# Kernel optimization log

Measured on AMD Instinct MI355X. Metric: run time of the kernel, lower is better.

## Reference

```python
import jax, jax.numpy as jnp
import numpy as np

# dims
B, C, N, E = 2048, 3, 32, 256       # batch, views, keypoints, embed_dim
H, L, MLP, P = 8, 3, 1024, 256      # heads, blocks (depth-1), mlp hidden, proj_dim
VIS_KP = 16                          # visible keypoints per sample (constant, as the torch code assumes)
K = VIS_KP + 1                       # + always-visible view token
HD = E // H
SCALE = HD ** -0.5


def _sinusoidal_pe(n, d):
    pos = np.arange(n)[:, None].astype(np.float32)
    i = np.arange(d)[None, :]
    ang = pos / np.power(10000.0, (2 * (i // 2)) / d)
    pe = np.where(i % 2 == 0, np.sin(ang), np.cos(ang))
    return jnp.asarray(pe, dtype=jnp.float32)

PE = _sinusoidal_pe(N, E)  # (N, E)


def layer_norm(x, s, b, eps=1e-5):
    mu = jnp.mean(x, -1, keepdims=True)
    var = jnp.var(x, -1, keepdims=True)
    return (x - mu) * jax.lax.rsqrt(var + eps) * s + b


def _heads(t, T):
    return t.reshape(-1, T, H, HD).transpose(0, 2, 1, 3)  # (S,H,T,HD)


def _gelu(x):
    return jax.nn.gelu(x, approximate=False)


def _mha(x, qkv_w, qkv_b, pw, pb):
    T = x.shape[1]
    q, k, v = jnp.split(x @ qkv_w + qkv_b, 3, axis=-1)
    q, k, v = _heads(q, T), _heads(k, T), _heads(v, T)
    a = jax.nn.softmax(jnp.einsum('shtd,shud->shtu', q, k) * SCALE, -1)
    o = jnp.einsum('shtu,shud->shtd', a, v).transpose(0, 2, 1, 3).reshape(-1, T, E)
    return o @ pw + pb


def reference(x, occlusion_mask, kp_w, kp_b, view_tokens, view_pos,
              ln1_s, ln1_b, qkv_w, qkv_b, ap_w, ap_b, ln2_s, ln2_b,
              fc1_w, fc1_b, fc2_w, fc2_b,
              pool_probe, pool_ln1_s, pool_ln1_b, pool_q_w, pool_q_b,
              pool_kv_w, pool_kv_b, pool_ap_w, pool_ap_b,
              pool_ln2_s, pool_ln2_b, pool_fc1_w, pool_fc1_b,
              pool_fc2_w, pool_fc2_b, pool_out_w, pool_out_b, last_s, last_b):
    # keypoint embedding + sinusoidal positional encoding
    xe = x.reshape(B * C, N, 2) @ kp_w + kp_b + PE[None]
    xe = xe.reshape(B, C, N, E)
    # prepend learnable view tokens (+ view positional embedding)
    vt = jnp.broadcast_to(view_tokens + view_pos, (B, C, 1, E))
    xt = jnp.concatenate([vt, xe], axis=2).reshape(B * C, N + 1, E)
    mask = jnp.concatenate([jnp.ones((B, C, 1, 1), bool), occlusion_mask], axis=2)
    mask = mask.reshape(B * C, N + 1)
    # stream compaction: gather the K visible tokens per sample, order-preserving
    order = jnp.argsort(jnp.where(mask, 0, 1).astype(jnp.int32), axis=1)[:, :K]
    vis = jnp.take_along_axis(xt, order[:, :, None], axis=1)  # (B*C, K, E)
    # pre-norm transformer blocks
    for l in range(L):
        y = vis + _mha(layer_norm(vis, ln1_s[l], ln1_b[l]), qkv_w[l], qkv_b[l], ap_w[l], ap_b[l])
        h = _gelu(layer_norm(y, ln2_s[l], ln2_b[l]) @ fc1_w[l] + fc1_b[l]) @ fc2_w[l] + fc2_b[l]
        vis = y + h
    # attention pooling: learnable probe cross-attends to the sequence
    probe = jnp.broadcast_to(pool_probe, (B * C, 1, E))
    kn = layer_norm(vis, pool_ln1_s, pool_ln1_b)
    q = _heads(probe @ pool_q_w + pool_q_b, 1)
    kk, vv = jnp.split(kn @ pool_kv_w + pool_kv_b, 2, axis=-1)
    kk, vv = _heads(kk, K), _heads(vv, K)
    a = jax.nn.softmax(jnp.einsum('shqd,shkd->shqk', q, kk) * SCALE, -1)
    o = jnp.einsum('shqk,shkd->shqd', a, vv).transpose(0, 2, 1, 3).reshape(B * C, 1, E)
    y = probe + o @ pool_ap_w + pool_ap_b
    y = y + _gelu(layer_norm(y, pool_ln2_s, pool_ln2_b) @ pool_fc1_w + pool_fc1_b) @ pool_fc2_w + pool_fc2_b
    out = (y @ pool_out_w + pool_out_b).reshape(B, C, P)
    return layer_norm(out, last_s, last_b)


def setup_inputs() -> dict:
    key = jax.random.key(0)
    ks = iter(jax.random.split(key, 64))

    def rn(shape, scale=0.02):
        return jax.random.normal(next(ks), shape, jnp.float32) * scale

    x = jax.random.normal(next(ks), (B, C, N, 2), jnp.float32)
    # exactly VIS_KP visible keypoints per sample (torch code assumes constant count)
    rng = np.random.default_rng(0)
    r = rng.random((B, C, N))
    rank = np.argsort(np.argsort(r, axis=-1), axis=-1)
    occlusion_mask = jnp.asarray((rank < VIS_KP)[..., None])
    return dict(
        x=x, occlusion_mask=occlusion_mask,
        kp_w=rn((2, E)), kp_b=jnp.zeros((E,)),
        view_tokens=rn((1, C, 1, E)), view_pos=rn((1, C, 1, E)),
        ln1_s=jnp.ones((L, E)), ln1_b=jnp.zeros((L, E)),
        qkv_w=rn((L, E, 3 * E)), qkv_b=jnp.zeros((L, 3 * E)),
        ap_w=rn((L, E, E)), ap_b=jnp.zeros((L, E)),
        ln2_s=jnp.ones((L, E)), ln2_b=jnp.zeros((L, E)),
        fc1_w=rn((L, E, MLP)), fc1_b=jnp.zeros((L, MLP)),
        fc2_w=rn((L, MLP, E)), fc2_b=jnp.zeros((L, E)),
        pool_probe=rn((1, 1, E)),
        pool_ln1_s=jnp.ones((E,)), pool_ln1_b=jnp.zeros((E,)),
        pool_q_w=rn((E, E)), pool_q_b=jnp.zeros((E,)),
        pool_kv_w=rn((E, 2 * E)), pool_kv_b=jnp.zeros((2 * E,)),
        pool_ap_w=rn((E, E)), pool_ap_b=jnp.zeros((E,)),
        pool_ln2_s=jnp.ones((E,)), pool_ln2_b=jnp.zeros((E,)),
        pool_fc1_w=rn((E, MLP)), pool_fc1_b=jnp.zeros((MLP,)),
        pool_fc2_w=rn((MLP, E)), pool_fc2_b=jnp.zeros((E,)),
        pool_out_w=rn((E, P)), pool_out_b=jnp.zeros((P,)),
        last_s=jnp.ones((P,)), last_b=jnp.zeros((P,)),
    )
```

## Files before the change

### kernel.cpp

```cpp
#include <hip/hip_runtime.h>
#include <hip/hip_bf16.h>
#include <math.h>


#define NB   2048
#define NC   3
#define NN   32
#define NE   256
#define NH   8
#define HDIM 32
#define NL   3
#define NMLP 1024
#define NP   256
#define NK   17
#define NR   (2*NK)
#define NS   (NB*NC)
#define NBLK (NS/2)
#define NT   512
#define NW   8
#define AST  264
#define BHS  520
#define BVS  260

#define SZ_QKV  589824
#define SZ_AP   196608
#define SZ_FC1  786432
#define SZ_FC2  786432
#define SZ_KV   131072
#define OFF_QKV 0
#define OFF_AP  (OFF_QKV + SZ_QKV)
#define OFF_FC1 (OFF_AP + SZ_AP)
#define OFF_FC2 (OFF_FC1 + SZ_FC1)
#define OFF_KV  (OFF_FC2 + SZ_FC2)
#define WTOT    (OFF_KV + SZ_KV)
#define WS_NEEDED ((size_t)WTOT * 2 * 2)

typedef unsigned short u16;
typedef __attribute__((ext_vector_type(8))) short short8;
typedef __attribute__((ext_vector_type(4))) float float4v;

struct Params {
  const void* x; const void* mask;
  const void* kp_w; const void* kp_b;
  const void* view_tokens; const void* view_pos;
  const void* ln1_s; const void* ln1_b;
  const void* qkv_w; const void* qkv_b;
  const void* ap_w; const void* ap_b;
  const void* ln2_s; const void* ln2_b;
  const void* fc1_w; const void* fc1_b;
  const void* fc2_w; const void* fc2_b;
  const void* pool_probe;
  const void* pool_ln1_s; const void* pool_ln1_b;
  const void* pool_q_w; const void* pool_q_b;
  const void* pool_kv_w; const void* pool_kv_b;
  const void* pool_ap_w; const void* pool_ap_b;
  const void* pool_ln2_s; const void* pool_ln2_b;
  const void* pool_fc1_w; const void* pool_fc1_b;
  const void* pool_fc2_w; const void* pool_fc2_b;
  const void* pool_out_w; const void* pool_out_b;
  const void* last_s; const void* last_b;
  float* out;
  u16* ws;
};

__device__ __forceinline__ float b2f(u16 u) {
  return __uint_as_float(((unsigned)u) << 16);
}
__device__ __forceinline__ u16 cvt16(float v) {
  return __bfloat16_as_ushort(__float2bfloat16(v));
}
__device__ __forceinline__ float geluf(float v) {
  return 0.5f * v * (1.0f + erff(v * 0.70710678118654752f));
}
template <bool BF>
__device__ __forceinline__ float LD(const void* q, int i) {
  if constexpr (BF) return b2f(((const u16*)q)[i]);
  else return ((const float*)q)[i];
}
__device__ __forceinline__ float4v vzero() {
  float4v z; z[0] = 0.f; z[1] = 0.f; z[2] = 0.f; z[3] = 0.f; return z;
}

template <bool BF>
__device__ void prep_body(const Params& p, int idx) {
  size_t i = idx, src; const void* W;
  if (i < SZ_QKV) {
    const size_t l = i / 196608, r = i % 196608, n = r / 256, k = r % 256;
    W = p.qkv_w; src = l * 196608 + k * 768 + n;
  } else if ((i -= SZ_QKV) < SZ_AP) {
    const size_t l = i / 65536, r = i % 65536, n = r / 256, k = r % 256;
    W = p.ap_w; src = l * 65536 + k * 256 + n;
  } else if ((i -= SZ_AP) < SZ_FC1) {
    const size_t l = i / 262144, r = i % 262144, n = r / 256, k = r % 256;
    W = p.fc1_w; src = l * 262144 + k * 1024 + n;
  } else if ((i -= SZ_FC1) < SZ_FC2) {
    const size_t l = i / 262144, r = i % 262144, n = r / 1024, k = r % 1024;
    W = p.fc2_w; src = l * 262144 + k * 256 + n;
  } else {
    i -= SZ_FC2;
    const size_t n = i / 256, k = i % 256;
    W = p.pool_kv_w; src = k * 512 + n;
  }
  u16 hi, lo;
  if constexpr (BF) {
    hi = ((const u16*)W)[src]; lo = 0;
  } else {
    const float wv = ((const float*)W)[src];
    hi = cvt16(wv);
    lo = cvt16(wv - b2f(hi));
  }
  p.ws[idx] = hi;
  p.ws[WTOT + idx] = lo;
}

__global__ __launch_bounds__(256)
void prep_kernel(Params p) {
  const int idx = blockIdx.x * 256 + threadIdx.x;
  if (idx >= WTOT) return;
  const bool isbf = (((const u16*)p.ln1_s)[0] == 0x3F80);
  if (isbf) prep_body<true>(p, idx);
  else      prep_body<false>(p, idx);
}

struct alignas(16) Smem {
  float X[NR][NE];
  u16  Ahi[NR * AST];
  u16  Alo[NR * AST];
  u16  Bh[NR * BHS];
  float Bv[NR][BVS];
  float Q[2][NE];
  float O[2][NE];
  float RowA[2][NE];
  float Pp[2][NH][NK];
  float Red[NW];
  int  Idx[2][NK];
};

template <bool BF>
__device__ __forceinline__ void ln_hl(const float* __restrict__ In,
                                      u16* __restrict__ Oh, u16* __restrict__ Ol,
                                      const void* __restrict__ gam,
                                      const void* __restrict__ bet) {
  const int lane = threadIdx.x & 63, w = threadIdx.x >> 6;
  for (int t = w; t < NR; t += NW) {
    const float* row = In + t * NE;
    float sum = 0.f, sq = 0.f;
#pragma unroll
    for (int kk = 0; kk < NE / 64; ++kk) {
      const float v = row[lane + 64 * kk];
      sum += v; sq += v * v;
    }
#pragma unroll
    for (int off = 32; off > 0; off >>= 1) {
      sum += __shfl_down(sum, off, 64);
      sq  += __shfl_down(sq,  off, 64);
    }
    sum = __shfl(sum, 0, 64);
    sq  = __shfl(sq,  0, 64);
    const float mu = sum * (1.0f / NE);
    const float r  = rsqrtf(sq * (1.0f / NE) - mu * mu + 1e-5f);
#pragma unroll
    for (int kk = 0; kk < NE / 64; ++kk) {
      const int k = lane + 64 * kk;
      const float v = (row[k] - mu) * r * LD<BF>(gam, k) + LD<BF>(bet, k);
      const u16 hv = cvt16(v);
      Oh[t * AST + k] = hv;
      Ol[t * AST + k] = cvt16(v - b2f(hv));
    }
  }
}

template <bool BF>
__device__ __forceinline__ void tile9(const short8 f0h, const short8 f0l,
                                      const short8 f1h, const short8 f1l,
                                      const short8 a2h, const short8 a2l,
                                      const short8 bh, const short8 bl,
                                      float4v& D0, float4v& D1, float4v& D2) {
  D0 = __builtin_amdgcn_mfma_f32_16x16x32_bf16(f0h, bh, D0, 0, 0, 0);
  D1 = __builtin_amdgcn_mfma_f32_16x16x32_bf16(f1h, bh, D1, 0, 0, 0);
  D2 = __builtin_amdgcn_mfma_f32_16x16x32_bf16(a2h, bh, D2, 0, 0, 0);
  D0 = __builtin_amdgcn_mfma_f32_16x16x32_bf16(f0l, bh, D0, 0, 0, 0);
  D1 = __builtin_amdgcn_mfma_f32_16x16x32_bf16(f1l, bh, D1, 0, 0, 0);
  D2 = __builtin_amdgcn_mfma_f32_16x16x32_bf16(a2l, bh, D2, 0, 0, 0);
  if constexpr (!BF) {
    D0 = __builtin_amdgcn_mfma_f32_16x16x32_bf16(f0h, bl, D0, 0, 0, 0);
    D1 = __builtin_amdgcn_mfma_f32_16x16x32_bf16(f1h, bl, D1, 0, 0, 0);
    D2 = __builtin_amdgcn_mfma_f32_16x16x32_bf16(a2h, bl, D2, 0, 0, 0);
  }
}

template <bool BF, int KS, int KST>
__device__ __forceinline__ void mfmaD_ws(const u16* __restrict__ Ah,
                                         const u16* __restrict__ Al,
                                         const int ast,
                                         const u16* __restrict__ Wh,
                                         const u16* __restrict__ Wl,
                                         const int koff,
                                         const int n0, const int n1,
                                         float4v& D0a, float4v& D1a, float4v& D2a,
                                         float4v& D0b, float4v& D1b, float4v& D2b) {
  const int lane = threadIdx.x & 63;
  const int col = lane & 15, quad = lane >> 4;
  const u16* __restrict__ b0h = Wh + (size_t)n0 * KST + koff + quad * 8;
  const u16* __restrict__ b0l = Wl + (size_t)n0 * KST + koff + quad * 8;
  const u16* __restrict__ b1h = Wh + (size_t)n1 * KST + koff + quad * 8;
  const u16* __restrict__ b1l = Wl + (size_t)n1 * KST + koff + quad * 8;
  const short8 z8 = {0, 0, 0, 0, 0, 0, 0, 0};
#pragma unroll
  for (int ks = 0; ks < KS; ++ks) {
    const int k0 = ks * 32 + quad * 8;
    const short8 bh0 = *(const short8*)(b0h + ks * 32);
    const short8 bh1 = *(const short8*)(b1h + ks * 32);
    short8 bl0 = z8, bl1 = z8;
    if constexpr (!BF) {
      bl0 = *(const short8*)(b0l + ks * 32);
      bl1 = *(const short8*)(b1l + ks * 32);
    }
    const short8 f0h = *(const short8*)(Ah + col * ast + k0);
    const short8 f0l = *(const short8*)(Al + col * ast + k0);
    const short8 f1h = *(const short8*)(Ah + (16 + col) * ast + k0);
    const short8 f1l = *(const short8*)(Al + (16 + col) * ast + k0);
    short8 a2h = z8, a2l = z8;
    if (col < 2) {
      a2h = *(const short8*)(Ah + (32 + col) * ast + k0);
      a2l = *(const short8*)(Al + (32 + col) * ast + k0);
    }
    tile9<BF>(f0h, f0l, f1h, f1l, a2h, a2l, bh0, bl0, D0a, D1a, D2a);
    tile9<BF>(f0h, f0l, f1h, f1l, a2h, a2l, bh1, bl1, D0b, D1b, D2b);
  }
}

template <bool BF, int KS, int KST>
__device__ __forceinline__ void mfmaT_ws(const u16* __restrict__ Ah,
                                         const u16* __restrict__ Al,
                                         const int ast,
                                         const u16* __restrict__ Wh,
                                         const u16* __restrict__ Wl,
                                         const int koff,
                                         const int n0, const int n1, const int n2,
                                         float4v& D0a, float4v& D1a, float4v& D2a,
                                         float4v& D0b, float4v& D1b, float4v& D2b,
                                         float4v& D0c, float4v& D1c, float4v& D2c) {
  const int lane = threadIdx.x & 63;
  const int col = lane & 15, quad = lane >> 4;
  const u16* __restrict__ b0h = Wh + (size_t)n0 * KST + koff + quad * 8;
  const u16* __restrict__ b0l = Wl + (size_t)n0 * KST + koff + quad * 8;
  const u16* __restrict__ b1h = Wh + (size_t)n1 * KST + koff + quad * 8;
  const u16* __restrict__ b1l = Wl + (size_t)n1 * KST + koff + quad * 8;
  const u16* __restrict__ b2h = Wh + (size_t)n2 * KST + koff + quad * 8;
  const u16* __restrict__ b2l = Wl + (size_t)n2 * KST + koff + quad * 8;
  const short8 z8 = {0, 0, 0, 0, 0, 0, 0, 0};
#pragma unroll
  for (int ks = 0; ks < KS; ++ks) {
    const int k0 = ks * 32 + quad * 8;
    const short8 f0h = *(const short8*)(Ah + col * ast + k0);
    const short8 f0l = *(const short8*)(Al + col * ast + k0);
    const short8 f1h = *(const short8*)(Ah + (16 + col) * ast + k0);
    const short8 f1l = *(const short8*)(Al + (16 + col) * ast + k0);
    short8 a2h = z8, a2l = z8;
    if (col < 2) {
      a2h = *(const short8*)(Ah + (32 + col) * ast + k0);
      a2l = *(const short8*)(Al + (32 + col) * ast + k0);
    }
    {
      const short8 bh0 = *(const short8*)(b0h + ks * 32);
      const short8 bh1 = *(const short8*)(b1h + ks * 32);
      short8 bl0 = z8, bl1 = z8;
      if constexpr (!BF) {
        bl0 = *(const short8*)(b0l + ks * 32);
        bl1 = *(const short8*)(b1l + ks * 32);
      }
      tile9<BF>(f0h, f0l, f1h, f1l, a2h, a2l, bh0, bl0, D0a, D1a, D2a);
      tile9<BF>(f0h, f0l, f1h, f1l, a2h, a2l, bh1, bl1, D0b, D1b, D2b);
    }
    {
      const short8 bh2 = *(const short8*)(b2h + ks * 32);
      short8 bl2 = z8;
      if constexpr (!BF) bl2 = *(const short8*)(b2l + ks * 32);
      tile9<BF>(f0h, f0l, f1h, f1l, a2h, a2l, bh2, bl2, D0c, D1c, D2c);
    }
  }
}

template <bool BF, int KS>
__device__ __forceinline__ void mfma1_in(const u16* __restrict__ Ah,
                                         const u16* __restrict__ Al,
                                         const int ast,
                                         const void* __restrict__ W, const int wN,
                                         const int koff, const int n,
                                         float4v& D0, float4v& D1, float4v& D2) {
  const int lane = threadIdx.x & 63;
  const int col = lane & 15, quad = lane >> 4;
  const short8 z8 = {0, 0, 0, 0, 0, 0, 0, 0};
  for (int ks = 0; ks < KS; ++ks) {
    const int k0 = ks * 32 + quad * 8;
    const short8 f0h = *(const short8*)(Ah + col * ast + k0);
    const short8 f0l = *(const short8*)(Al + col * ast + k0);
    const short8 f1h = *(const short8*)(Ah + (16 + col) * ast + k0);
    const short8 f1l = *(const short8*)(Al + (16 + col) * ast + k0);
    short8 a2h = z8, a2l = z8;
    if (col < 2) {
      a2h = *(const short8*)(Ah + (32 + col) * ast + k0);
      a2l = *(const short8*)(Al + (32 + col) * ast + k0);
    }
    short8 bh, bl = z8;
#pragma unroll
    for (int j2 = 0; j2 < 8; ++j2) {
      const size_t off = (size_t)(koff + k0 + j2) * wN + n;
      if constexpr (BF) {
        bh[j2] = (short)((const u16*)W)[off];
      } else {
        const float wv = ((const float*)W)[off];
        const u16 hv = cvt16(wv);
        bh[j2] = (short)hv;
        bl[j2] = (short)cvt16(wv - b2f(hv));
      }
    }
    tile9<BF>(f0h, f0l, f1h, f1l, a2h, a2l, bh, bl, D0, D1, D2);
  }
}

__device__ __forceinline__ float group_sum(float v, float* sRed, int sid) {
#pragma unroll
  for (int off = 32; off > 0; off >>= 1) v += __shfl_down(v, off, 64);
  __syncthreads();
  if ((threadIdx.x & 63) == 0) sRed[threadIdx.x >> 6] = v;
  __syncthreads();
  return sRed[sid * 4 + 0] + sRed[sid * 4 + 1] +
         sRed[sid * 4 + 2] + sRed[sid * 4 + 3];
}

template <bool BF, bool WS>
__device__ void body(const Params& p, Smem& sm) {
  const int s0  = blockIdx.x * 2;
  const int tid = threadIdx.x;
  const size_t EB = BF ? 2 : 4;
  const int lane = tid & 63, wv_ = tid >> 6, col = lane & 15, quad = lane >> 4;
  const u16* wsh = p.ws;
  const u16* wsl = p.ws + WTOT;
  u16* Hhi = sm.Bh;
  u16* Hlo = (u16*)&sm.Bv[0][0];

  if (tid < 2) {
    const int sid = tid, sg = s0 + sid;
    const unsigned int* mw = (const unsigned int*)p.mask;
    bool byte_layout = false;
    for (int i = 0; i < 8; ++i) {
      const unsigned int w = mw[i];
      if (w != 0u && w != 1u && w != 0x3F800000u) { byte_layout = true; break; }
    }
    int np_ = 0;
    sm.Idx[sid][np_++] = -1;
    if (byte_layout) {
      const unsigned char* mb = (const unsigned char*)p.mask;
      for (int n = 0; n < NN && np_ < NK; ++n)
        if (mb[(size_t)sg * NN + n]) sm.Idx[sid][np_++] = n;
    } else {
      for (int n = 0; n < NN && np_ < NK; ++n)
        if (mw[(size_t)sg * NN + n] != 0u) sm.Idx[sid][np_++] = n;
    }
    while (np_ < NK) sm.Idx[sid][np_++] = 0;
  }
  __syncthreads();

  {
    const int e  = tid & (NE - 1);
    const int th = tid >> 8;
    const float kw0 = LD<BF>(p.kp_w, e);
    const float kw1 = LD<BF>(p.kp_w, NE + e);
    const float kb  = LD<BF>(p.kp_b, e);
    const int   i2  = e & ~1;
    const float freq = expf(-((float)i2 / (float)NE) * logf(10000.0f));
    for (int g = th; g < NR; g += 2) {
      const int sid = (g >= NK) ? 1 : 0;
      const int t   = g - sid * NK;
      const int sg  = s0 + sid;
      const int c   = sg % NC;
      const int n   = sm.Idx[sid][t];
      float v;
      if (n < 0) {
        v = LD<BF>(p.view_tokens, c * NE + e) + LD<BF>(p.view_pos, c * NE + e);
      } else {
        const float x0 = LD<BF>(p.x, (sg * NN + n) * 2 + 0);
        const float x1 = LD<BF>(p.x, (sg * NN + n) * 2 + 1);
        const float ang = (float)n * freq;
        const float pe  = (e & 1) ? cosf(ang) : sinf(ang);
        v = x0 * kw0 + x1 * kw1 + kb + pe;
      }
      sm.X[g][e] = v;
    }
  }
  __syncthreads();

#pragma unroll 1
  for (int l = 0; l < NL; ++l) {
    const void* qkvw = (const char*)p.qkv_w + (size_t)l * NE * 3 * NE * EB;
    const void* qkvb = (const char*)p.qkv_b + (size_t)l * 3 * NE * EB;
    const void* apw  = (const char*)p.ap_w  + (size_t)l * NE * NE * EB;
    const void* apb  = (const char*)p.ap_b  + (size_t)l * NE * EB;
    const void* f1w  = (const char*)p.fc1_w + (size_t)l * NE * NMLP * EB;
    const void* f1b  = (const char*)p.fc1_b + (size_t)l * NMLP * EB;
    const void* f2w  = (const char*)p.fc2_w + (size_t)l * NMLP * NE * EB;
    const void* f2bb = (const char*)p.fc2_b + (size_t)l * NE * EB;

    ln_hl<BF>(&sm.X[0][0], sm.Ahi, sm.Alo,
              (const char*)p.ln1_s + (size_t)l * NE * EB,
              (const char*)p.ln1_b + (size_t)l * NE * EB);
    __syncthreads();

    {
      auto wb_qkv = [&](int n, float4v D0, float4v D1, float4v D2) {
        const float bb = LD<BF>(qkvb, n);
#pragma unroll
        for (int r = 0; r < 4; ++r) {
          const int g0 = quad * 4 + r;
          const int g1 = 16 + quad * 4 + r;
          const int g2 = 32 + quad * 4 + r;
          if (n < 512) {
            sm.Bh[g0 * BHS + n] = cvt16(D0[r] + bb);
            sm.Bh[g1 * BHS + n] = cvt16(D1[r] + bb);
            if (g2 < NR) sm.Bh[g2 * BHS + n] = cvt16(D2[r] + bb);
          } else {
            sm.Bv[g0][n - 512] = D0[r] + bb;
            sm.Bv[g1][n - 512] = D1[r] + bb;
            if (g2 < NR) sm.Bv[g2][n - 512] = D2[r] + bb;
          }
        }
      };
#pragma unroll 1
      for (int pass = 0; pass < 2; ++pass) {
        const int n0 = (wv_ + (pass * 3 + 0) * NW) * 16 + col;
        const int n1 = (wv_ + (pass * 3 + 1) * NW) * 16 + col;
        const int n2 = (wv_ + (pass * 3 + 2) * NW) * 16 + col;
        float4v D0a = vzero(), D1a = vzero(), D2a = vzero();
        float4v D0b = vzero(), D1b = vzero(), D2b = vzero();
        float4v D0c = vzero(), D1c = vzero(), D2c = vzero();
        if constexpr (WS)
          mfmaT_ws<BF, 8, 256>(sm.Ahi, sm.Alo, AST,
                               wsh + OFF_QKV + (size_t)l * 196608,
                               wsl + OFF_QKV + (size_t)l * 196608, 0,
                               n0, n1, n2,
                               D0a, D1a, D2a, D0b, D1b, D2b, D0c, D1c, D2c);
        else {
          mfma1_in<BF, 8>(sm.Ahi, sm.Alo, AST, qkvw, 3 * NE, 0, n0, D0a, D1a, D2a);
          mfma1_in<BF, 8>(sm.Ahi, sm.Alo, AST, qkvw, 3 * NE, 0, n1, D0b, D1b, D2b);
          mfma1_in<BF, 8>(sm.Ahi, sm.Alo, AST, qkvw, 3 * NE, 0, n2, D0c, D1c, D2c);
        }
        wb_qkv(n0, D0a, D1a, D2a);
        wb_qkv(n1, D0b, D1b, D2b);
        wb_qkv(n2, D0c, D1c, D2c);
      }
    }
    __syncthreads();

    if (tid < 2 * NH * NK) {
      const int sid = tid / (NH * NK);
      const int rem = tid - sid * (NH * NK);
      const int h = rem / NK, t = rem % NK;
      const int gb = sid * NK;
      float q[HDIM];
#pragma unroll
      for (int i8 = 0; i8 < HDIM / 8; ++i8) {
        const short8 qq = *(const short8*)&sm.Bh[(gb + t) * BHS + h * HDIM + i8 * 8];
#pragma unroll
        for (int j = 0; j < 8; ++j) q[i8 * 8 + j] = b2f((u16)qq[j]);
      }
      float sc[NK];
      float mx = -1e30f;
#pragma unroll
      for (int u = 0; u < NK; ++u) {
        float d = 0.f;
#pragma unroll
        for (int i8 = 0; i8 < HDIM / 8; ++i8) {
          const short8 kk = *(const short8*)&sm.Bh[(gb + u) * BHS + 256 + h * HDIM + i8 * 8];
#pragma unroll
          for (int j = 0; j < 8; ++j) d += q[i8 * 8 + j] * b2f((u16)kk[j]);
        }
        d *= 0.17677669529663687f;
        sc[u] = d;
        mx = fmaxf(mx, d);
      }
      float den = 0.f;
#pragma unroll
      for (int u = 0; u < NK; ++u) { sc[u] = __expf(sc[u] - mx); den += sc[u]; }
      const float inv = 1.0f / den;
#pragma unroll
      for (int u = 0; u < NK; ++u) sc[u] *= inv;
#pragma unroll
      for (int i4 = 0; i4 < HDIM / 4; ++i4) {
        float4v o = vzero();
#pragma unroll
        for (int u = 0; u < NK; ++u) {
          const float4v vv = *(const float4v*)&sm.Bv[gb + u][h * HDIM + i4 * 4];
          o[0] += sc[u] * vv[0];
          o[1] += sc[u] * vv[1];
          o[2] += sc[u] * vv[2];
          o[3] += sc[u] * vv[3];
        }
#pragma unroll
        for (int r = 0; r < 4; ++r) {
          const int jc = h * HDIM + i4 * 4 + r;
          const u16 hv = cvt16(o[r]);
          sm.Ahi[(gb + t) * AST + jc] = hv;
          sm.Alo[(gb + t) * AST + jc] = cvt16(o[r] - b2f(hv));
        }
      }
    }
    __syncthreads();

    {
      auto wb_proj = [&](int n, float4v D0, float4v D1, float4v D2) {
        const float bb = LD<BF>(apb, n);
#pragma unroll
        for (int r = 0; r < 4; ++r) {
          const int g0 = quad * 4 + r;
          const int g1 = 16 + quad * 4 + r;
          const int g2 = 32 + quad * 4 + r;
          sm.X[g0][n] = sm.X[g0][n] + D0[r] + bb;
          sm.X[g1][n] = sm.X[g1][n] + D1[r] + bb;
          if (g2 < NR) sm.X[g2][n] = sm.X[g2][n] + D2[r] + bb;
        }
      };
      const int n0 = wv_ * 16 + col;
      const int n1 = (wv_ + NW) * 16 + col;
      float4v D0a = vzero(), D1a = vzero(), D2a = vzero();
      float4v D0b = vzero(), D1b = vzero(), D2b = vzero();
      if constexpr (WS)
        mfmaD_ws<BF, 8, 256>(sm.Ahi, sm.Alo, AST,
                             wsh + OFF_AP + (size_t)l * 65536,
                             wsl + OFF_AP + (size_t)l * 65536, 0, n0, n1,
                             D0a, D1a, D2a, D0b, D1b, D2b);
      else {
        mfma1_in<BF, 8>(sm.Ahi, sm.Alo, AST, apw, NE, 0, n0, D0a, D1a, D2a);
        mfma1_in<BF, 8>(sm.Ahi, sm.Alo, AST, apw, NE, 0, n1, D0b, D1b, D2b);
      }
      wb_proj(n0, D0a, D1a, D2a);
      wb_proj(n1, D0b, D1b, D2b);
    }
    __syncthreads();

    ln_hl<BF>(&sm.X[0][0], sm.Ahi, sm.Alo,
              (const char*)p.ln2_s + (size_t)l * NE * EB,
              (const char*)p.ln2_b + (size_t)l * NE * EB);
    __syncthreads();

#pragma unroll 1
    for (int chunk = 0; chunk < 2; ++chunk) {
      {
        auto wb_fc1 = [&](int n, float4v D0, float4v D1, float4v D2) {
          const float bb = LD<BF>(f1b, chunk * 512 + n);
#pragma unroll
          for (int r = 0; r < 4; ++r) {
            const int g0 = quad * 4 + r;
            const int g1 = 16 + quad * 4 + r;
            const int g2 = 32 + quad * 4 + r;
            {
              const float v = geluf(D0[r] + bb);
              const u16 hv = cvt16(v);
              Hhi[g0 * BHS + n] = hv;
              Hlo[g0 * BHS + n] = cvt16(v - b2f(hv));
            }
            {
              const float v = geluf(D1[r] + bb);
              const u16 hv = cvt16(v);
              Hhi[g1 * BHS + n] = hv;
              Hlo[g1 * BHS + n] = cvt16(v - b2f(hv));
            }
            if (g2 < NR) {
              const float v = geluf(D2[r] + bb);
              const u16 hv = cvt16(v);
              Hhi[g2 * BHS + n] = hv;
              Hlo[g2 * BHS + n] = cvt16(v - b2f(hv));
            }
          }
        };
#pragma unroll 1
        for (int pass = 0; pass < 2; ++pass) {
          const int n0 = (wv_ + (pass * 2 + 0) * NW) * 16 + col;
          const int n1 = (wv_ + (pass * 2 + 1) * NW) * 16 + col;
          float4v D0a = vzero(), D1a = vzero(), D2a = vzero();
          float4v D0b = vzero(), D1b = vzero(), D2b = vzero();
          if constexpr (WS)
            mfmaD_ws<BF, 8, 256>(sm.Ahi, sm.Alo, AST,
                                 wsh + OFF_FC1 + (size_t)l * 262144 + (size_t)chunk * 131072,
                                 wsl + OFF_FC1 + (size_t)l * 262144 + (size_t)chunk * 131072,
                                 0, n0, n1, D0a, D1a, D2a, D0b, D1b, D2b);
          else {
            const void* f1wc = (const char*)f1w + (size_t)chunk * 512 * EB;
            mfma1_in<BF, 8>(sm.Ahi, sm.Alo, AST, f1wc, NMLP, 0, n0, D0a, D1a, D2a);
            mfma1_in<BF, 8>(sm.Ahi, sm.Alo, AST, f1wc, NMLP, 0, n1, D0b, D1b, D2b);
          }
          wb_fc1(n0, D0a, D1a, D2a);
          wb_fc1(n1, D0b, D1b, D2b);
        }
      }
      __syncthreads();
      {
        auto wb_fc2 = [&](int n, float4v D0, float4v D1, float4v D2) {
          const float bb = (chunk == 0) ? LD<BF>(f2bb, n) : 0.f;
#pragma unroll
          for (int r = 0; r < 4; ++r) {
            const int g0 = quad * 4 + r;
            const int g1 = 16 + quad * 4 + r;
            const int g2 = 32 + quad * 4 + r;
            sm.X[g0][n] = sm.X[g0][n] + D0[r] + bb;
            sm.X[g1][n] = sm.X[g1][n] + D1[r] + bb;
            if (g2 < NR) sm.X[g2][n] = sm.X[g2][n] + D2[r] + bb;
          }
        };
        const int n0 = wv_ * 16 + col;
        const int n1 = (wv_ + NW) * 16 + col;
        float4v D0a = vzero(), D1a = vzero(), D2a = vzero();
        float4v D0b = vzero(), D1b = vzero(), D2b = vzero();
        if constexpr (WS)
          mfmaD_ws<BF, 16, 1024>(Hhi, Hlo, BHS,
                                 wsh + OFF_FC2 + (size_t)l * 262144,
                                 wsl + OFF_FC2 + (size_t)l * 262144,
                                 chunk * 512, n0, n1,
                                 D0a, D1a, D2a, D0b, D1b, D2b);
        else {
          mfma1_in<BF, 16>(Hhi, Hlo, BHS, f2w, NE, chunk * 512, n0, D0a, D1a, D2a);
          mfma1_in<BF, 16>(Hhi, Hlo, BHS, f2w, NE, chunk * 512, n1, D0b, D1b, D2b);
        }
        wb_fc2(n0, D0a, D1a, D2a);
        wb_fc2(n1, D0b, D1b, D2b);
      }
      __syncthreads();
    }
  }

  ln_hl<BF>(&sm.X[0][0], sm.Ahi, sm.Alo, p.pool_ln1_s, p.pool_ln1_b);
  __syncthreads();
  const int sid = tid >> 8;
  const int j   = tid & (NE - 1);
  {
    float a = LD<BF>(p.pool_q_b, j);
#pragma unroll 4
    for (int k = 0; k < NE; k += 4) {
      a += LD<BF>(p.pool_probe, k + 0) * LD<BF>(p.pool_q_w, (k + 0) * NE + j) +
           LD<BF>(p.pool_probe, k + 1) * LD<BF>(p.pool_q_w, (k + 1) * NE + j) +
           LD<BF>(p.pool_probe, k + 2) * LD<BF>(p.pool_q_w, (k + 2) * NE + j) +
           LD<BF>(p.pool_probe, k + 3) * LD<BF>(p.pool_q_w, (k + 3) * NE + j);
    }
    sm.Q[sid][j] = a;
  }
  {
    auto wb_kv = [&](int n, float4v D0, float4v D1, float4v D2) {
      const float bb = LD<BF>(p.pool_kv_b, n);
#pragma unroll
      for (int r = 0; r < 4; ++r) {
        const int g0 = quad * 4 + r;
        const int g1 = 16 + quad * 4 + r;
        const int g2 = 32 + quad * 4 + r;
        if (n < 256) {
          sm.Bh[g0 * BHS + n] = cvt16(D0[r] + bb);
          sm.Bh[g1 * BHS + n] = cvt16(D1[r] + bb);
          if (g2 < NR) sm.Bh[g2 * BHS + n] = cvt16(D2[r] + bb);
        } else {
          sm.Bv[g0][n - 256] = D0[r] + bb;
          sm.Bv[g1][n - 256] = D1[r] + bb;
          if (g2 < NR) sm.Bv[g2][n - 256] = D2[r] + bb;
        }
      }
    };
#pragma unroll 1
    for (int pass = 0; pass < 2; ++pass) {
      const int n0 = (wv_ + (pass * 2 + 0) * NW) * 16 + col;
      const int n1 = (wv_ + (pass * 2 + 1) * NW) * 16 + col;
      float4v D0a = vzero(), D1a = vzero(), D2a = vzero();
      float4v D0b = vzero(), D1b = vzero(), D2b = vzero();
      if constexpr (WS)
        mfmaD_ws<BF, 8, 256>(sm.Ahi, sm.Alo, AST, wsh + OFF_KV, wsl + OFF_KV,
                             0, n0, n1, D0a, D1a, D2a, D0b, D1b, D2b);
      else {
        mfma1_in<BF, 8>(sm.Ahi, sm.Alo, AST, p.pool_kv_w, 2 * NE, 0, n0, D0a, D1a, D2a);
        mfma1_in<BF, 8>(sm.Ahi, sm.Alo, AST, p.pool_kv_w, 2 * NE, 0, n1, D0b, D1b, D2b);
      }
      wb_kv(n0, D0a, D1a, D2a);
      wb_kv(n1, D0b, D1b, D2b);
    }
  }
  __syncthreads();
  if (tid < 2 * NH) {
    const int ps = tid >> 3, h = tid & 7;
    const int gb = ps * NK;
    float sc[NK];
    float mx = -1e30f;
#pragma unroll
    for (int u = 0; u < NK; ++u) {
      float d = 0.f;
#pragma unroll
      for (int i8 = 0; i8 < HDIM / 8; ++i8) {
        const short8 kk = *(const short8*)&sm.Bh[(gb + u) * BHS + h * HDIM + i8 * 8];
#pragma unroll
        for (int jx = 0; jx < 8; ++jx)
          d += sm.Q[ps][h * HDIM + i8 * 8 + jx] * b2f((u16)kk[jx]);
      }
      d *= 0.17677669529663687f;
      sc[u] = d;
      mx = fmaxf(mx, d);
    }
    float den = 0.f;
#pragma unroll
    for (int u = 0; u < NK; ++u) { sc[u] = __expf(sc[u] - mx); den += sc[u]; }
    const float inv = 1.0f / den;
#pragma unroll
    for (int u = 0; u < NK; ++u) sm.Pp[ps][h][u] = sc[u] * inv;
  }
  __syncthreads();
  {
    const int h = j >> 5, i = j & 31;
    float o = 0.f;
#pragma unroll
    for (int u = 0; u < NK; ++u)
      o += sm.Pp[sid][h][u] * sm.Bv[sid * NK + u][h * HDIM + i];
    sm.O[sid][j] = o;
  }
  __syncthreads();
  float yv;
  {
    float a = LD<BF>(p.pool_ap_b, j);
#pragma unroll 4
    for (int k = 0; k < NE; k += 4) {
      const float4 oo = *(const float4*)&sm.O[sid][k];
      a += oo.x * LD<BF>(p.pool_ap_w, (k + 0) * NE + j) +
           oo.y * LD<BF>(p.pool_ap_w, (k + 1) * NE + j) +
           oo.z * LD<BF>(p.pool_ap_w, (k + 2) * NE + j) +
           oo.w * LD<BF>(p.pool_ap_w, (k + 3) * NE + j);
    }
    yv = LD<BF>(p.pool_probe, j) + a;
  }
  {
    const float s1 = group_sum(yv, sm.Red, sid);
    const float s2 = group_sum(yv * yv, sm.Red, sid);
    const float mu = s1 * (1.0f / NE);
    const float r  = rsqrtf(s2 * (1.0f / NE) - mu * mu + 1e-5f);
    sm.Q[sid][j] = (yv - mu) * r * LD<BF>(p.pool_ln2_s, j) + LD<BF>(p.pool_ln2_b, j);
  }
  __syncthreads();
  float* Hh = (float*)&sm.Bv[0][0];
  {
    float h1[4];
#pragma unroll
    for (int c4 = 0; c4 < 4; ++c4) h1[c4] = LD<BF>(p.pool_fc1_b, c4 * NE + j);
#pragma unroll 4
    for (int k = 0; k < NE; k += 4) {
      const float4 nq = *(const float4*)&sm.Q[sid][k];
#pragma unroll
      for (int c4 = 0; c4 < 4; ++c4) {
        const int cjj = c4 * NE + j;
        h1[c4] += nq.x * LD<BF>(p.pool_fc1_w, (k + 0) * NMLP + cjj) +
                  nq.y * LD<BF>(p.pool_fc1_w, (k + 1) * NMLP + cjj) +
                  nq.z * LD<BF>(p.pool_fc1_w, (k + 2) * NMLP + cjj) +
                  nq.w * LD<BF>(p.pool_fc1_w, (k + 3) * NMLP + cjj);
      }
    }
    __syncthreads();
#pragma unroll
    for (int c4 = 0; c4 < 4; ++c4) Hh[sid * NMLP + c4 * NE + j] = geluf(h1[c4]);
  }
  __syncthreads();
  {
    float a = LD<BF>(p.pool_fc2_b, j);
#pragma unroll 4
    for (int k = 0; k < NMLP; k += 4) {
      const float4 hh = *(const float4*)&Hh[sid * NMLP + k];
      a += hh.x * LD<BF>(p.pool_fc2_w, (k + 0) * NE + j) +
           hh.y * LD<BF>(p.pool_fc2_w, (k + 1) * NE + j) +
           hh.z * LD<BF>(p.pool_fc2_w, (k + 2) * NE + j) +
           hh.w * LD<BF>(p.pool_fc2_w, (k + 3) * NE + j);
    }
    yv += a;
    sm.RowA[sid][j] = yv;
  }
  __syncthreads();
  float ov;
  {
    float a = LD<BF>(p.pool_out_b, j);
#pragma unroll 4
    for (int k = 0; k < NE; k += 4) {
      const float4 yy = *(const float4*)&sm.RowA[sid][k];
      a += yy.x * LD<BF>(p.pool_out_w, (k + 0) * NP + j) +
           yy.y * LD<BF>(p.pool_out_w, (k + 1) * NP + j) +
           yy.z * LD<BF>(p.pool_out_w, (k + 2) * NP + j) +
           yy.w * LD<BF>(p.pool_out_w, (k + 3) * NP + j);
    }
    ov = a;
  }
  {
    const float s1 = group_sum(ov, sm.Red, sid);
    const float s2 = group_sum(ov * ov, sm.Red, sid);
    const float mu = s1 * (1.0f / NP);
    const float r  = rsqrtf(s2 * (1.0f / NP) - mu * mu + 1e-5f);
    const float res = (ov - mu) * r * LD<BF>(p.last_s, j) + LD<BF>(p.last_b, j);
    p.out[(size_t)(s0 + sid) * NP + j] = res;
  }
}

__global__ __launch_bounds__(NT)
__attribute__((amdgpu_waves_per_eu(2, 2)))
void st_encoder_ws(Params p) {
  __shared__ Smem sm;
  const bool isbf = (((const u16*)p.ln1_s)[0] == 0x3F80);
  if (isbf) body<true, true>(p, sm);
  else      body<false, true>(p, sm);
}

__global__ __launch_bounds__(NT)
__attribute__((amdgpu_waves_per_eu(2, 2)))
void st_encoder_nows(Params p) {
  __shared__ Smem sm;
  const bool isbf = (((const u16*)p.ln1_s)[0] == 0x3F80);
  if (isbf) body<true, false>(p, sm);
  else      body<false, false>(p, sm);
}

extern "C" void kernel_launch(void* const* d_in, const int* in_sizes, int n_in,
                              void* d_out, int out_size, void* d_ws, size_t ws_size,
                              hipStream_t stream) {
  (void)in_sizes; (void)n_in; (void)out_size;
  Params p;
  p.x           = d_in[0];
  p.mask        = d_in[1];
  p.kp_w        = d_in[2];
  p.kp_b        = d_in[3];
  p.view_tokens = d_in[4];
  p.view_pos    = d_in[5];
  p.ln1_s       = d_in[6];
  p.ln1_b       = d_in[7];
  p.qkv_w       = d_in[8];
  p.qkv_b       = d_in[9];
  p.ap_w        = d_in[10];
  p.ap_b        = d_in[11];
  p.ln2_s       = d_in[12];
  p.ln2_b       = d_in[13];
  p.fc1_w       = d_in[14];
  p.fc1_b       = d_in[15];
  p.fc2_w       = d_in[16];
  p.fc2_b       = d_in[17];
  p.pool_probe  = d_in[18];
  p.pool_ln1_s  = d_in[19];
  p.pool_ln1_b  = d_in[20];
  p.pool_q_w    = d_in[21];
  p.pool_q_b    = d_in[22];
  p.pool_kv_w   = d_in[23];
  p.pool_kv_b   = d_in[24];
  p.pool_ap_w   = d_in[25];
  p.pool_ap_b   = d_in[26];
  p.pool_ln2_s  = d_in[27];
  p.pool_ln2_b  = d_in[28];
  p.pool_fc1_w  = d_in[29];
  p.pool_fc1_b  = d_in[30];
  p.pool_fc2_w  = d_in[31];
  p.pool_fc2_b  = d_in[32];
  p.pool_out_w  = d_in[33];
  p.pool_out_b  = d_in[34];
  p.last_s      = d_in[35];
  p.last_b      = d_in[36];
  p.out         = (float*)d_out;
  p.ws          = (u16*)d_ws;
  if (d_ws != nullptr && ws_size >= WS_NEEDED) {
    prep_kernel<<<dim3((WTOT + 255) / 256), dim3(256), 0, stream>>>(p);
    st_encoder_ws<<<dim3(NBLK), dim3(NT), 0, stream>>>(p);
  } else {
    st_encoder_nows<<<dim3(NBLK), dim3(NT), 0, stream>>>(p);
  }
}
```

Baseline: 5.257 ms.

## Double block size to 1024 threads and split MFMA tiles across sixteen waves

Raises threads per block from 512 to 1024 (16 waves) and redistributes the QKV, projection, FC1, FC2 and pool KV MFMA column tiles so each wave does one pass instead of two. A new single-column MFMA helper is added for the projection and FC2 stages. The pooling tail keeps its 512-thread mapping and guards the upper half of the block as inactive. The waves_per_eu hint is removed. The intent is more in-flight waves per block to hide latency, at the cost of higher register pressure per thread and idle waves during pooling.

```diff
diff --git a/kernel.cpp b/kernel.cpp
--- a/kernel.cpp
+++ b/kernel.cpp
@@ -16,8 +16,8 @@
 #define NR   (2*NK)
 #define NS   (NB*NC)
 #define NBLK (NS/2)
-#define NT   512
-#define NW   8
+#define NT   1024
+#define NW   16
 #define AST  264
 #define BHS  520
 #define BVS  260
@@ -190,6 +190,38 @@
 }
 
 template <bool BF, int KS, int KST>
+__device__ __forceinline__ void mfmaS_ws(const u16* __restrict__ Ah,
+                                         const u16* __restrict__ Al,
+                                         const int ast,
+                                         const u16* __restrict__ Wh,
+                                         const u16* __restrict__ Wl,
+                                         const int koff, const int n,
+                                         float4v& D0, float4v& D1, float4v& D2) {
+  const int lane = threadIdx.x & 63;
+  const int col = lane & 15, quad = lane >> 4;
+  const u16* __restrict__ b0h = Wh + (size_t)n * KST + koff + quad * 8;
+  const u16* __restrict__ b0l = Wl + (size_t)n * KST + koff + quad * 8;
+  const short8 z8 = {0, 0, 0, 0, 0, 0, 0, 0};
+#pragma unroll
+  for (int ks = 0; ks < KS; ++ks) {
+    const int k0 = ks * 32 + quad * 8;
+    const short8 bh0 = *(const short8*)(b0h + ks * 32);
+    short8 bl0 = z8;
+    if constexpr (!BF) bl0 = *(const short8*)(b0l + ks * 32);
+    const short8 f0h = *(const short8*)(Ah + col * ast + k0);
+    const short8 f0l = *(const short8*)(Al + col * ast + k0);
+    const short8 f1h = *(const short8*)(Ah + (16 + col) * ast + k0);
+    const short8 f1l = *(const short8*)(Al + (16 + col) * ast + k0);
+    short8 a2h = z8, a2l = z8;
+    if (col < 2) {
+      a2h = *(const short8*)(Ah + (32 + col) * ast + k0);
+      a2l = *(const short8*)(Al + (32 + col) * ast + k0);
+    }
+    tile9<BF>(f0h, f0l, f1h, f1l, a2h, a2l, bh0, bl0, D0, D1, D2);
+  }
+}
+
+template <bool BF, int KS, int KST>
 __device__ __forceinline__ void mfmaD_ws(const u16* __restrict__ Ah,
                                          const u16* __restrict__ Al,
                                          const int ast,
@@ -326,8 +358,8 @@
   __syncthreads();
   if ((threadIdx.x & 63) == 0) sRed[threadIdx.x >> 6] = v;
   __syncthreads();
-  return sRed[sid * 4 + 0] + sRed[sid * 4 + 1] +
-         sRed[sid * 4 + 2] + sRed[sid * 4 + 3];
+  const int b = (sid & 1) * 4;
+  return sRed[b + 0] + sRed[b + 1] + sRed[b + 2] + sRed[b + 3];
 }
 
 template <bool BF, bool WS>
@@ -371,7 +403,7 @@
     const float kb  = LD<BF>(p.kp_b, e);
     const int   i2  = e & ~1;
     const float freq = expf(-((float)i2 / (float)NE) * logf(10000.0f));
-    for (int g = th; g < NR; g += 2) {
+    for (int g = th; g < NR; g += 4) {
       const int sid = (g >= NK) ? 1 : 0;
       const int t   = g - sid * NK;
       const int sg  = s0 + sid;
@@ -427,29 +459,26 @@
           }
         }
       };
-#pragma unroll 1
-      for (int pass = 0; pass < 2; ++pass) {
-        const int n0 = (wv_ + (pass * 3 + 0) * NW) * 16 + col;
-        const int n1 = (wv_ + (pass * 3 + 1) * NW) * 16 + col;
-        const int n2 = (wv_ + (pass * 3 + 2) * NW) * 16 + col;
-        float4v D0a = vzero(), D1a = vzero(), D2a = vzero();
-        float4v D0b = vzero(), D1b = vzero(), D2b = vzero();
-        float4v D0c = vzero(), D1c = vzero(), D2c = vzero();
-        if constexpr (WS)
-          mfmaT_ws<BF, 8, 256>(sm.Ahi, sm.Alo, AST,
-                               wsh + OFF_QKV + (size_t)l * 196608,
-                               wsl + OFF_QKV + (size_t)l * 196608, 0,
-                               n0, n1, n2,
-                               D0a, D1a, D2a, D0b, D1b, D2b, D0c, D1c, D2c);
-        else {
-          mfma1_in<BF, 8>(sm.Ahi, sm.Alo, AST, qkvw, 3 * NE, 0, n0, D0a, D1a, D2a);
-          mfma1_in<BF, 8>(sm.Ahi, sm.Alo, AST, qkvw, 3 * NE, 0, n1, D0b, D1b, D2b);
-          mfma1_in<BF, 8>(sm.Ahi, sm.Alo, AST, qkvw, 3 * NE, 0, n2, D0c, D1c, D2c);
-        }
-        wb_qkv(n0, D0a, D1a, D2a);
-        wb_qkv(n1, D0b, D1b, D2b);
-        wb_qkv(n2, D0c, D1c, D2c);
-      }
+      const int n0 = (wv_ + 0 * NW) * 16 + col;
+      const int n1 = (wv_ + 1 * NW) * 16 + col;
+      const int n2 = (wv_ + 2 * NW) * 16 + col;
+      float4v D0a = vzero(), D1a = vzero(), D2a = vzero();
+      float4v D0b = vzero(), D1b = vzero(), D2b = vzero();
+      float4v D0c = vzero(), D1c = vzero(), D2c = vzero();
+      if constexpr (WS)
+        mfmaT_ws<BF, 8, 256>(sm.Ahi, sm.Alo, AST,
+                             wsh + OFF_QKV + (size_t)l * 196608,
+                             wsl + OFF_QKV + (size_t)l * 196608, 0,
+                             n0, n1, n2,
+                             D0a, D1a, D2a, D0b, D1b, D2b, D0c, D1c, D2c);
+      else {
+        mfma1_in<BF, 8>(sm.Ahi, sm.Alo, AST, qkvw, 3 * NE, 0, n0, D0a, D1a, D2a);
+        mfma1_in<BF, 8>(sm.Ahi, sm.Alo, AST, qkvw, 3 * NE, 0, n1, D0b, D1b, D2b);
+        mfma1_in<BF, 8>(sm.Ahi, sm.Alo, AST, qkvw, 3 * NE, 0, n2, D0c, D1c, D2c);
+      }
+      wb_qkv(n0, D0a, D1a, D2a);
+      wb_qkv(n1, D0b, D1b, D2b);
+      wb_qkv(n2, D0c, D1c, D2c);
     }
     __syncthreads();
 
@@ -522,20 +551,15 @@
         }
       };
       const int n0 = wv_ * 16 + col;
-      const int n1 = (wv_ + NW) * 16 + col;
       float4v D0a = vzero(), D1a = vzero(), D2a = vzero();
-      float4v D0b = vzero(), D1b = vzero(), D2b = vzero();
       if constexpr (WS)
-        mfmaD_ws<BF, 8, 256>(sm.Ahi, sm.Alo, AST,
+        mfmaS_ws<BF, 8, 256>(sm.Ahi, sm.Alo, AST,
                              wsh + OFF_AP + (size_t)l * 65536,
-                             wsl + OFF_AP + (size_t)l * 65536, 0, n0, n1,
-                             D0a, D1a, D2a, D0b, D1b, D2b);
-      else {
+                             wsl + OFF_AP + (size_t)l * 65536, 0, n0,
+                             D0a, D1a, D2a);
+      else
         mfma1_in<BF, 8>(sm.Ahi, sm.Alo, AST, apw, NE, 0, n0, D0a, D1a, D2a);
-        mfma1_in<BF, 8>(sm.Ahi, sm.Alo, AST, apw, NE, 0, n1, D0b, D1b, D2b);
-      }
       wb_proj(n0, D0a, D1a, D2a);
-      wb_proj(n1, D0b, D1b, D2b);
     }
     __syncthreads();
 
@@ -574,25 +598,22 @@
             }
           }
         };
-#pragma unroll 1
-        for (int pass = 0; pass < 2; ++pass) {
-          const int n0 = (wv_ + (pass * 2 + 0) * NW) * 16 + col;
-          const int n1 = (wv_ + (pass * 2 + 1) * NW) * 16 + col;
-          float4v D0a = vzero(), D1a = vzero(), D2a = vzero();
-          float4v D0b = vzero(), D1b = vzero(), D2b = vzero();
-          if constexpr (WS)
-            mfmaD_ws<BF, 8, 256>(sm.Ahi, sm.Alo, AST,
-                                 wsh + OFF_FC1 + (size_t)l * 262144 + (size_t)chunk * 131072,
-                                 wsl + OFF_FC1 + (size_t)l * 262144 + (size_t)chunk * 131072,
-                                 0, n0, n1, D0a, D1a, D2a, D0b, D1b, D2b);
-          else {
-            const void* f1wc = (const char*)f1w + (size_t)chunk * 512 * EB;
-            mfma1_in<BF, 8>(sm.Ahi, sm.Alo, AST, f1wc, NMLP, 0, n0, D0a, D1a, D2a);
-            mfma1_in<BF, 8>(sm.Ahi, sm.Alo, AST, f1wc, NMLP, 0, n1, D0b, D1b, D2b);
-          }
-          wb_fc1(n0, D0a, D1a, D2a);
-          wb_fc1(n1, D0b, D1b, D2b);
+        const int n0 = (wv_ + 0 * NW) * 16 + col;
+        const int n1 = (wv_ + 1 * NW) * 16 + col;
+        float4v D0a = vzero(), D1a = vzero(), D2a = vzero();
+        float4v D0b = vzero(), D1b = vzero(), D2b = vzero();
+        if constexpr (WS)
+          mfmaD_ws<BF, 8, 256>(sm.Ahi, sm.Alo, AST,
+                               wsh + OFF_FC1 + (size_t)l * 262144 + (size_t)chunk * 131072,
+                               wsl + OFF_FC1 + (size_t)l * 262144 + (size_t)chunk * 131072,
+                               0, n0, n1, D0a, D1a, D2a, D0b, D1b, D2b);
+        else {
+          const void* f1wc = (const char*)f1w + (size_t)chunk * 512 * EB;
+          mfma1_in<BF, 8>(sm.Ahi, sm.Alo, AST, f1wc, NMLP, 0, n0, D0a, D1a, D2a);
+          mfma1_in<BF, 8>(sm.Ahi, sm.Alo, AST, f1wc, NMLP, 0, n1, D0b, D1b, D2b);
         }
+        wb_fc1(n0, D0a, D1a, D2a);
+        wb_fc1(n1, D0b, D1b, D2b);
       }
       __syncthreads();
       {
@@ -609,21 +630,15 @@
           }
         };
         const int n0 = wv_ * 16 + col;
-        const int n1 = (wv_ + NW) * 16 + col;
         float4v D0a = vzero(), D1a = vzero(), D2a = vzero();
-        float4v D0b = vzero(), D1b = vzero(), D2b = vzero();
         if constexpr (WS)
-          mfmaD_ws<BF, 16, 1024>(Hhi, Hlo, BHS,
+          mfmaS_ws<BF, 16, 1024>(Hhi, Hlo, BHS,
                                  wsh + OFF_FC2 + (size_t)l * 262144,
                                  wsl + OFF_FC2 + (size_t)l * 262144,
-                                 chunk * 512, n0, n1,
-                                 D0a, D1a, D2a, D0b, D1b, D2b);
-        else {
+                                 chunk * 512, n0, D0a, D1a, D2a);
+        else
           mfma1_in<BF, 16>(Hhi, Hlo, BHS, f2w, NE, chunk * 512, n0, D0a, D1a, D2a);
-          mfma1_in<BF, 16>(Hhi, Hlo, BHS, f2w, NE, chunk * 512, n1, D0b, D1b, D2b);
-        }
         wb_fc2(n0, D0a, D1a, D2a);
-        wb_fc2(n1, D0b, D1b, D2b);
       }
       __syncthreads();
     }
@@ -631,9 +646,10 @@
 
   ln_hl<BF>(&sm.X[0][0], sm.Ahi, sm.Alo, p.pool_ln1_s, p.pool_ln1_b);
   __syncthreads();
-  const int sid = tid >> 8;
+  const int sid = (tid >> 8) & 1;
   const int j   = tid & (NE - 1);
-  {
+  const bool pool_act = (tid < 512);
+  if (pool_act) {
     float a = LD<BF>(p.pool_q_b, j);
 #pragma unroll 4
     for (int k = 0; k < NE; k += 4) {
@@ -663,22 +679,19 @@
         }
       }
     };
-#pragma unroll 1
-    for (int pass = 0; pass < 2; ++pass) {
-      const int n0 = (wv_ + (pass * 2 + 0) * NW) * 16 + col;
-      const int n1 = (wv_ + (pass * 2 + 1) * NW) * 16 + col;
-      float4v D0a = vzero(), D1a = vzero(), D2a = vzero();
-      float4v D0b = vzero(), D1b = vzero(), D2b = vzero();
-      if constexpr (WS)
-        mfmaD_ws<BF, 8, 256>(sm.Ahi, sm.Alo, AST, wsh + OFF_KV, wsl + OFF_KV,
-                             0, n0, n1, D0a, D1a, D2a, D0b, D1b, D2b);
-      else {
-        mfma1_in<BF, 8>(sm.Ahi, sm.Alo, AST, p.pool_kv_w, 2 * NE, 0, n0, D0a, D1a, D2a);
-        mfma1_in<BF, 8>(sm.Ahi, sm.Alo, AST, p.pool_kv_w, 2 * NE, 0, n1, D0b, D1b, D2b);
-      }
-      wb_kv(n0, D0a, D1a, D2a);
-      wb_kv(n1, D0b, D1b, D2b);
-    }
+    const int n0 = (wv_ + 0 * NW) * 16 + col;
+    const int n1 = (wv_ + 1 * NW) * 16 + col;
+    float4v D0a = vzero(), D1a = vzero(), D2a = vzero();
+    float4v D0b = vzero(), D1b = vzero(), D2b = vzero();
+    if constexpr (WS)
+      mfmaD_ws<BF, 8, 256>(sm.Ahi, sm.Alo, AST, wsh + OFF_KV, wsl + OFF_KV,
+                           0, n0, n1, D0a, D1a, D2a, D0b, D1b, D2b);
+    else {
+      mfma1_in<BF, 8>(sm.Ahi, sm.Alo, AST, p.pool_kv_w, 2 * NE, 0, n0, D0a, D1a, D2a);
+      mfma1_in<BF, 8>(sm.Ahi, sm.Alo, AST, p.pool_kv_w, 2 * NE, 0, n1, D0b, D1b, D2b);
+    }
+    wb_kv(n0, D0a, D1a, D2a);
+    wb_kv(n1, D0b, D1b, D2b);
   }
   __syncthreads();
   if (tid < 2 * NH) {
@@ -708,7 +721,7 @@
     for (int u = 0; u < NK; ++u) sm.Pp[ps][h][u] = sc[u] * inv;
   }
   __syncthreads();
-  {
+  if (pool_act) {
     const int h = j >> 5, i = j & 31;
     float o = 0.f;
 #pragma unroll
@@ -717,8 +730,8 @@
     sm.O[sid][j] = o;
   }
   __syncthreads();
-  float yv;
-  {
+  float yv = 0.f;
+  if (pool_act) {
     float a = LD<BF>(p.pool_ap_b, j);
 #pragma unroll 4
     for (int k = 0; k < NE; k += 4) {
@@ -731,36 +744,41 @@
     yv = LD<BF>(p.pool_probe, j) + a;
   }
   {
-    const float s1 = group_sum(yv, sm.Red, sid);
-    const float s2 = group_sum(yv * yv, sm.Red, sid);
+    const float s1 = group_sum(pool_act ? yv : 0.f, sm.Red, sid);
+    const float s2 = group_sum(pool_act ? yv * yv : 0.f, sm.Red, sid);
     const float mu = s1 * (1.0f / NE);
     const float r  = rsqrtf(s2 * (1.0f / NE) - mu * mu + 1e-5f);
-    sm.Q[sid][j] = (yv - mu) * r * LD<BF>(p.pool_ln2_s, j) + LD<BF>(p.pool_ln2_b, j);
+    if (pool_act)
+      sm.Q[sid][j] = (yv - mu) * r * LD<BF>(p.pool_ln2_s, j) + LD<BF>(p.pool_ln2_b, j);
   }
   __syncthreads();
   float* Hh = (float*)&sm.Bv[0][0];
   {
     float h1[4];
-#pragma unroll
-    for (int c4 = 0; c4 < 4; ++c4) h1[c4] = LD<BF>(p.pool_fc1_b, c4 * NE + j);
+    if (pool_act) {
+#pragma unroll
+      for (int c4 = 0; c4 < 4; ++c4) h1[c4] = LD<BF>(p.pool_fc1_b, c4 * NE + j);
 #pragma unroll 4
-    for (int k = 0; k < NE; k += 4) {
-      const float4 nq = *(const float4*)&sm.Q[sid][k];
-#pragma unroll
-      for (int c4 = 0; c4 < 4; ++c4) {
-        const int cjj = c4 * NE + j;
-        h1[c4] += nq.x * LD<BF>(p.pool_fc1_w, (k + 0) * NMLP + cjj) +
-                  nq.y * LD<BF>(p.pool_fc1_w, (k + 1) * NMLP + cjj) +
-                  nq.z * LD<BF>(p.pool_fc1_w, (k + 2) * NMLP + cjj) +
-                  nq.w * LD<BF>(p.pool_fc1_w, (k + 3) * NMLP + cjj);
+      for (int k = 0; k < NE; k += 4) {
+        const float4 nq = *(const float4*)&sm.Q[sid][k];
+#pragma unroll
+        for (int c4 = 0; c4 < 4; ++c4) {
+          const int cjj = c4 * NE + j;
+          h1[c4] += nq.x * LD<BF>(p.pool_fc1_w, (k + 0) * NMLP + cjj) +
+                    nq.y * LD<BF>(p.pool_fc1_w, (k + 1) * NMLP + cjj) +
+                    nq.z * LD<BF>(p.pool_fc1_w, (k + 2) * NMLP + cjj) +
+                    nq.w * LD<BF>(p.pool_fc1_w, (k + 3) * NMLP + cjj);
+        }
       }
     }
     __syncthreads();
-#pragma unroll
-    for (int c4 = 0; c4 < 4; ++c4) Hh[sid * NMLP + c4 * NE + j] = geluf(h1[c4]);
-  }
-  __syncthreads();
-  {
+    if (pool_act) {
+#pragma unroll
+      for (int c4 = 0; c4 < 4; ++c4) Hh[sid * NMLP + c4 * NE + j] = geluf(h1[c4]);
+    }
+  }
+  __syncthreads();
+  if (pool_act) {
     float a = LD<BF>(p.pool_fc2_b, j);
 #pragma unroll 4
     for (int k = 0; k < NMLP; k += 4) {
@@ -774,8 +792,8 @@
     sm.RowA[sid][j] = yv;
   }
   __syncthreads();
-  float ov;
-  {
+  float ov = 0.f;
+  if (pool_act) {
     float a = LD<BF>(p.pool_out_b, j);
 #pragma unroll 4
     for (int k = 0; k < NE; k += 4) {
@@ -788,17 +806,18 @@
     ov = a;
   }
   {
-    const float s1 = group_sum(ov, sm.Red, sid);
-    const float s2 = group_sum(ov * ov, sm.Red, sid);
+    const float s1 = group_sum(pool_act ? ov : 0.f, sm.Red, sid);
+    const float s2 = group_sum(pool_act ? ov * ov : 0.f, sm.Red, sid);
     const float mu = s1 * (1.0f / NP);
     const float r  = rsqrtf(s2 * (1.0f / NP) - mu * mu + 1e-5f);
-    const float res = (ov - mu) * r * LD<BF>(p.last_s, j) + LD<BF>(p.last_b, j);
-    p.out[(size_t)(s0 + sid) * NP + j] = res;
+    if (pool_act) {
+      const float res = (ov - mu) * r * LD<BF>(p.last_s, j) + LD<BF>(p.last_b, j);
+      p.out[(size_t)(s0 + sid) * NP + j] = res;
+    }
   }
 }
 
 __global__ __launch_bounds__(NT)
-__attribute__((amdgpu_waves_per_eu(2, 2)))
 void st_encoder_ws(Params p) {
   __shared__ Smem sm;
   const bool isbf = (((const u16*)p.ln1_s)[0] == 0x3F80);
@@ -807,7 +826,6 @@
 }
 
 __global__ __launch_bounds__(NT)
-__attribute__((amdgpu_waves_per_eu(2, 2)))
 void st_encoder_nows(Params p) {
   __shared__ Smem sm;
   const bool isbf = (((const u16*)p.ln1_s)[0] == 0x3F80);
```

Measured after the change: 6.200 ms. 1.18x slower.
